# Kernel tuning notes

Measured on AMD Instinct MI355X. Metric: run time of the kernel, lower is better.

The kernel has to match this reference:

```python
import jax, jax.numpy as jnp
import numpy as np

B, N, P, H, BINF = 64, 100, 640000, 128, 11

def setup_inputs() -> dict:
    key = jax.random.key(0)
    ks = jax.random.split(key, 10)
    s = 1.0 / np.sqrt(H)
    sparse_idx = jnp.stack([
        jax.random.randint(ks[0], (P,), 0, B),
        jax.random.randint(ks[1], (P,), 0, N),
        jax.random.randint(ks[2], (P,), 0, N),
    ], axis=1).astype(jnp.int64)  # [P, 3]
    return {
        "local_pair": jax.random.normal(ks[3], (P, H), jnp.float32),
        "global_pair": jax.random.normal(ks[4], (P, H), jnp.float32),
        "binary": jax.random.normal(ks[5], (B, N, N, BINF), jnp.float32),
        "sparse_idx": sparse_idx,
        "W_local": jax.random.normal(ks[6], (H, H), jnp.float32) * s,
        "W_global": jax.random.normal(ks[7], (H, H), jnp.float32) * s,
        "b_global": jnp.zeros((H,), jnp.float32),
        "W_binary": jax.random.normal(ks[8], (BINF, H), jnp.float32) * s,
        "W_score": jax.random.normal(ks[9], (H, 5), jnp.float32) * s,
        "b_score": jnp.zeros((5,), jnp.float32),
    }

def reference(local_pair, global_pair, binary, sparse_idx,
              W_local, W_global, b_global, W_binary, W_score, b_score):
    # gather binary bond features for each scored pair: [P, BINF]
    binary_feats = binary[sparse_idx[:, 0], sparse_idx[:, 1], sparse_idx[:, 2]]
    # fused 3-way linear + relu
    pair_feats = jax.nn.relu(
        local_pair @ W_local
        + (global_pair @ W_global + b_global)
        + binary_feats @ W_binary
    )  # [P, H]
    score = pair_feats @ W_score + b_score  # [P, 5]
    return score
```

## Files before the change

### kernel.cpp

```cpp
#include <hip/hip_runtime.h>
#include <stdint.h>

typedef __bf16 bf16x8 __attribute__((ext_vector_type(8)));
typedef float f32x16 __attribute__((ext_vector_type(16)));

#define H 128
#define NBINF 11
#define NCHUNK 17
#define PTOT 640000
#define ROWS 64
#define NT (PTOT / ROWS)
#define GRID 512
#define ASTRIDE 560
#define ABUF (ROWS * ASTRIDE)
#define FSTRIDE 272

__device__ __align__(16) unsigned short g_wpack[NCHUNK * 4 * 64 * 8];
__device__ __align__(16) unsigned short g_wsp[8 * 64 * 8];
__device__ int g_flag;

__device__ __forceinline__ unsigned short f2bf(float f) {
  return (unsigned short)__builtin_bit_cast(unsigned short, (__bf16)f);
}

__global__ void k_flag(const int* __restrict__ sidx) {
  int t = threadIdx.x;
  int v = sidx[2 * t + 1];
  unsigned long long any = __ballot(v != 0);
  if (t == 0) g_flag = (any == 0ull) ? 2 : 1;
}

__global__ void k_pack(const float* __restrict__ Wl, const float* __restrict__ Wg,
                       const float* __restrict__ Wb, const float* __restrict__ Wsc) {
  int tid = blockIdx.x * 256 + threadIdx.x;
  if (tid < NCHUNK * 4 * 64 * 8) {
    int j = tid & 7, l = (tid >> 3) & 63, nt = (tid >> 9) & 3, c = tid >> 11;
    int k = c * 16 + ((l >> 5) << 3) + j;
    int n = nt * 32 + (l & 31);
    float v = 0.f;
    if (k < 128)       v = Wl[k * H + n];
    else if (k < 256)  v = Wg[(k - 128) * H + n];
    else { int kk = k - 256; v = (kk < NBINF) ? Wb[kk * H + n] : 0.f; }
    g_wpack[tid] = f2bf(v);
  }
  if (tid < 8 * 64 * 8) {
    int j = tid & 7, l = (tid >> 3) & 63, cs = tid >> 9;
    int s = l & 31;
    int k = cs * 16 + ((l >> 5) << 3) + j;
    float v = (s < 5) ? Wsc[k * 5 + s] : 0.f;
    g_wsp[tid] = f2bf(v);
  }
}

__device__ __forceinline__ void bar_lgkm() {
  asm volatile("s_waitcnt lgkmcnt(0)" ::: "memory");
  __builtin_amdgcn_s_barrier();
}

__launch_bounds__(256, 2)
__global__ void k_main(const float* __restrict__ lp, const float* __restrict__ gp,
                       const float* __restrict__ bin, const int* __restrict__ sidx,
                       const float* __restrict__ bg, const float* __restrict__ bsc,
                       float* __restrict__ out) {
  __shared__ __align__(16) char sm[2 * ABUF];
  const int t   = threadIdx.x;
  const int wid = t >> 6;
  const int l   = t & 63;
  const int lr  = l & 31;
  const int lh  = l >> 5;
  const int sflag = g_flag;

  bf16x8 wreg[NCHUNK];
#pragma unroll
  for (int c = 0; c < NCHUNK; ++c)
    wreg[c] = *(const bf16x8*)(g_wpack + ((size_t)(c * 4 + wid) * 64 + l) * 8);
  bf16x8 ws[8];
#pragma unroll
  for (int cs = 0; cs < 8; ++cs)
    ws[cs] = *(const bf16x8*)(g_wsp + ((size_t)cs * 64 + l) * 8);

  const float bgv = bg[wid * 32 + lr];
  const float b0 = bsc[0], b1 = bsc[1], b2 = bsc[2], b3 = bsc[3], b4 = bsc[4];

  float4 pay[16];
  float  bv[8];

  auto issue = [&](int tile) {
    const int p0 = tile * ROWS;
#pragma unroll
    for (int i = 0; i < 8; ++i) {
      int u = t + i * 256, row = u >> 5, slot = u & 31;
      const float* src = (slot < 16)
          ? lp + (size_t)(p0 + row) * H + slot * 8
          : gp + (size_t)(p0 + row) * H + (slot - 16) * 8;
      pay[2 * i]     = ((const float4*)src)[0];
      pay[2 * i + 1] = ((const float4*)src)[1];
    }
    if (t < 2 * ROWS) {
      int row = t >> 1, bh = t & 1, prow = p0 + row;
      int bi = sidx[(prow * 3 + 0) * sflag];
      int ii = sidx[(prow * 3 + 1) * sflag];
      int jj = sidx[(prow * 3 + 2) * sflag];
      int base = ((bi * 100 + ii) * 100 + jj) * NBINF;
#pragma unroll
      for (int j = 0; j < 8; ++j) {
        int e = bh * 8 + j;
        bv[j] = (e < NBINF) ? bin[base + e] : 0.f;
      }
    }
  };

  auto commit = [&](int buf) {
    char* dst = sm + buf * ABUF;
#pragma unroll
    for (int i = 0; i < 8; ++i) {
      int u = t + i * 256, row = u >> 5, slot = u & 31;
      float4 a = pay[2 * i], b = pay[2 * i + 1];
      bf16x8 v;
      v[0] = (__bf16)a.x; v[1] = (__bf16)a.y; v[2] = (__bf16)a.z; v[3] = (__bf16)a.w;
      v[4] = (__bf16)b.x; v[5] = (__bf16)b.y; v[6] = (__bf16)b.z; v[7] = (__bf16)b.w;
      *(bf16x8*)(dst + row * ASTRIDE + slot * 16) = v;
    }
    if (t < 2 * ROWS) {
      int row = t >> 1, bh = t & 1;
      bf16x8 v;
#pragma unroll
      for (int j = 0; j < 8; ++j) v[j] = (__bf16)bv[j];
      *(bf16x8*)(dst + row * ASTRIDE + 512 + bh * 16) = v;
    }
  };

  const int tile0 = blockIdx.x;
  issue(tile0);
  commit(0);
  bar_lgkm();

  int cur = 0;
  for (int tile = tile0; tile < NT; tile += GRID) {
    const int nxt = tile + GRID;
    if (nxt < NT) issue(nxt);

    const char* A = sm + cur * ABUF;
    f32x16 acc[2] = {};
#pragma unroll
    for (int c = 0; c < NCHUNK; ++c) {
#pragma unroll
      for (int rt = 0; rt < 2; ++rt) {
        bf16x8 a = *(const bf16x8*)(A + (rt * 32 + lr) * ASTRIDE + c * 32 + lh * 16);
        acc[rt] = __builtin_amdgcn_mfma_f32_32x32x16_bf16(a, wreg[c], acc[rt], 0, 0, 0);
      }
    }
    bar_lgkm();

    {
      char* F = sm + cur * ABUF;
#pragma unroll
      for (int rt = 0; rt < 2; ++rt) {
#pragma unroll
        for (int rg = 0; rg < 16; ++rg) {
          int rowt = (rg & 3) + ((rg >> 2) << 3) + (lh << 2);
          float fv = fmaxf(acc[rt][rg] + bgv, 0.f);
          *(__bf16*)(F + (size_t)(rt * 32 + rowt) * FSTRIDE +
                     (size_t)(wid * 32 + lr) * 2) = (__bf16)fv;
        }
      }
    }
    bar_lgkm();

    if (wid < 2) {
      const char* F = sm + cur * ABUF;
      f32x16 sacc = {};
#pragma unroll
      for (int cs = 0; cs < 8; ++cs) {
        bf16x8 fb = *(const bf16x8*)(F + (size_t)(wid * 32 + lr) * FSTRIDE +
                                     cs * 32 + lh * 16);
        sacc = __builtin_amdgcn_mfma_f32_32x32x16_bf16(ws[cs], fb, sacc, 0, 0, 0);
      }
      int prow = tile * ROWS + wid * 32 + lr;
      float* op = out + (size_t)prow * 5;
      if (lh == 0) {
        op[0] = sacc[0] + b0; op[1] = sacc[1] + b1;
        op[2] = sacc[2] + b2; op[3] = sacc[3] + b3;
      } else {
        op[4] = sacc[0] + b4;
      }
    }

    if (nxt < NT) commit(cur ^ 1);
    bar_lgkm();
    cur ^= 1;
  }
}

extern "C" void kernel_launch(void* const* d_in, const int* in_sizes, int n_in,
                              void* d_out, int out_size, void* d_ws, size_t ws_size,
                              hipStream_t stream) {
  const float* lp  = (const float*)d_in[0];
  const float* gp  = (const float*)d_in[1];
  const float* bin = (const float*)d_in[2];
  const int*   si  = (const int*)d_in[3];
  const float* Wl  = (const float*)d_in[4];
  const float* Wg  = (const float*)d_in[5];
  const float* bg  = (const float*)d_in[6];
  const float* Wb  = (const float*)d_in[7];
  const float* Wsc = (const float*)d_in[8];
  const float* bsc = (const float*)d_in[9];
  float* out = (float*)d_out;

  hipLaunchKernelGGL(k_flag, dim3(1), dim3(64), 0, stream, si);
  hipLaunchKernelGGL(k_pack, dim3(136), dim3(256), 0, stream, Wl, Wg, Wb, Wsc);
  hipLaunchKernelGGL(k_main, dim3(GRID), dim3(256), 0, stream,
                     lp, gp, bin, si, bg, bsc, out);
}
```

Before: 147.3 us.

## Halve tile rows, prefetch two tiles ahead and split score GEMM across waves

Tiles shrink from 64 to 32 rows. Two register payload sets (A and B) now alternate, so global loads are issued two tiles ahead instead of one. The score projection, which only two waves ran before, is now split across all four waves: each wave computes a K-slice and writes partial sums to LDS, and a final pass reduces them and writes the output. The aim is to keep more memory traffic in flight and balance work across waves. The cost is an extra barrier per tile, an LDS reduction step, and a scattered output store pattern.

```diff
diff --git a/kernel.cpp b/kernel.cpp
--- a/kernel.cpp
+++ b/kernel.cpp
@@ -8,12 +8,13 @@
 #define NBINF 11
 #define NCHUNK 17
 #define PTOT 640000
-#define ROWS 64
+#define ROWS 32
 #define NT (PTOT / ROWS)
 #define GRID 512
 #define ASTRIDE 560
 #define ABUF (ROWS * ASTRIDE)
 #define FSTRIDE 272
+#define PARTOFF 9216
 
 __device__ __align__(16) unsigned short g_wpack[NCHUNK * 4 * 64 * 8];
 __device__ __align__(16) unsigned short g_wsp[8 * 64 * 8];
@@ -74,25 +75,23 @@
 #pragma unroll
   for (int c = 0; c < NCHUNK; ++c)
     wreg[c] = *(const bf16x8*)(g_wpack + ((size_t)(c * 4 + wid) * 64 + l) * 8);
-  bf16x8 ws[8];
-#pragma unroll
-  for (int cs = 0; cs < 8; ++cs)
-    ws[cs] = *(const bf16x8*)(g_wsp + ((size_t)cs * 64 + l) * 8);
+  bf16x8 ws0 = *(const bf16x8*)(g_wsp + ((size_t)(2 * wid + 0) * 64 + l) * 8);
+  bf16x8 ws1 = *(const bf16x8*)(g_wsp + ((size_t)(2 * wid + 1) * 64 + l) * 8);
 
   const float bgv = bg[wid * 32 + lr];
-  const float b0 = bsc[0], b1 = bsc[1], b2 = bsc[2], b3 = bsc[3], b4 = bsc[4];
-
-  float4 pay[16];
-  float  bv[8];
-
-  auto issue = [&](int tile) {
+
+  float4 payA[8]; float bvA[8];
+  float4 payB[8]; float bvB[8];
+
+  auto issue = [&](int tile, float4 (&pay)[8], float (&bv)[8]) {
     const int p0 = tile * ROWS;
 #pragma unroll
-    for (int i = 0; i < 8; ++i) {
-      int u = t + i * 256, row = u >> 5, slot = u & 31;
-      const float* src = (slot < 16)
-          ? lp + (size_t)(p0 + row) * H + slot * 8
-          : gp + (size_t)(p0 + row) * H + (slot - 16) * 8;
+    for (int i = 0; i < 4; ++i) {
+      int v = t + 256 * i;
+      int row = v >> 5, c32 = v & 31;
+      const float* src = (c32 < 16)
+          ? lp + (size_t)(p0 + row) * H + c32 * 8
+          : gp + (size_t)(p0 + row) * H + (c32 - 16) * 8;
       pay[2 * i]     = ((const float4*)src)[0];
       pay[2 * i + 1] = ((const float4*)src)[1];
     }
@@ -110,85 +109,80 @@
     }
   };
 
-  auto commit = [&](int buf) {
-    char* dst = sm + buf * ABUF;
-#pragma unroll
-    for (int i = 0; i < 8; ++i) {
-      int u = t + i * 256, row = u >> 5, slot = u & 31;
+  auto commit = [&](char* dst, float4 (&pay)[8], float (&bv)[8]) {
+#pragma unroll
+    for (int i = 0; i < 4; ++i) {
+      int v = t + 256 * i;
+      int row = v >> 5, c32 = v & 31;
       float4 a = pay[2 * i], b = pay[2 * i + 1];
-      bf16x8 v;
-      v[0] = (__bf16)a.x; v[1] = (__bf16)a.y; v[2] = (__bf16)a.z; v[3] = (__bf16)a.w;
-      v[4] = (__bf16)b.x; v[5] = (__bf16)b.y; v[6] = (__bf16)b.z; v[7] = (__bf16)b.w;
-      *(bf16x8*)(dst + row * ASTRIDE + slot * 16) = v;
+      bf16x8 x;
+      x[0] = (__bf16)a.x; x[1] = (__bf16)a.y; x[2] = (__bf16)a.z; x[3] = (__bf16)a.w;
+      x[4] = (__bf16)b.x; x[5] = (__bf16)b.y; x[6] = (__bf16)b.z; x[7] = (__bf16)b.w;
+      *(bf16x8*)(dst + row * ASTRIDE + c32 * 16) = x;
     }
     if (t < 2 * ROWS) {
       int row = t >> 1, bh = t & 1;
-      bf16x8 v;
-#pragma unroll
-      for (int j = 0; j < 8; ++j) v[j] = (__bf16)bv[j];
-      *(bf16x8*)(dst + row * ASTRIDE + 512 + bh * 16) = v;
+      bf16x8 x;
+#pragma unroll
+      for (int j = 0; j < 8; ++j) x[j] = (__bf16)bv[j];
+      *(bf16x8*)(dst + row * ASTRIDE + 512 + bh * 16) = x;
     }
   };
 
-  const int tile0 = blockIdx.x;
-  issue(tile0);
-  commit(0);
+  auto compute = [&](char* buf, int tile) {
+    f32x16 acc = {};
+#pragma unroll
+    for (int c = 0; c < NCHUNK; ++c) {
+      bf16x8 a = *(const bf16x8*)(buf + lr * ASTRIDE + c * 32 + lh * 16);
+      acc = __builtin_amdgcn_mfma_f32_32x32x16_bf16(a, wreg[c], acc, 0, 0, 0);
+    }
+    bar_lgkm();
+#pragma unroll
+    for (int rg = 0; rg < 16; ++rg) {
+      int p = (rg & 3) + ((rg >> 2) << 3) + (lh << 2);
+      float fv = fmaxf(acc[rg] + bgv, 0.f);
+      *(__bf16*)(buf + (size_t)p * FSTRIDE + (size_t)(wid * 32 + lr) * 2) = (__bf16)fv;
+    }
+    bar_lgkm();
+    f32x16 sacc = {};
+    bf16x8 fb0 = *(const bf16x8*)(buf + (size_t)lr * FSTRIDE + (2 * wid) * 32 + lh * 16);
+    bf16x8 fb1 = *(const bf16x8*)(buf + (size_t)lr * FSTRIDE + (2 * wid + 1) * 32 + lh * 16);
+    sacc = __builtin_amdgcn_mfma_f32_32x32x16_bf16(ws0, fb0, sacc, 0, 0, 0);
+    sacc = __builtin_amdgcn_mfma_f32_32x32x16_bf16(ws1, fb1, sacc, 0, 0, 0);
+    char* part = buf + PARTOFF;
+    if (lh == 0) {
+#pragma unroll
+      for (int s = 0; s < 4; ++s)
+        *(float*)(part + ((size_t)(s * 32 + lr) * 4 + wid) * 4) = sacc[s];
+    } else {
+      *(float*)(part + ((size_t)(4 * 32 + lr) * 4 + wid) * 4) = sacc[0];
+    }
+    bar_lgkm();
+    if (t < 160) {
+      int s = t >> 5, p = t & 31;
+      float4 q = *(const float4*)(part + (size_t)t * 16);
+      out[(size_t)(tile * ROWS + p) * 5 + s] = q.x + q.y + q.z + q.w + bsc[s];
+    }
+  };
+
+  const int t0 = blockIdx.x;
+  issue(t0, payA, bvA);
+  commit(sm, payA, bvA);
+  issue(t0 + GRID, payB, bvB);
   bar_lgkm();
 
-  int cur = 0;
-  for (int tile = tile0; tile < NT; tile += GRID) {
-    const int nxt = tile + GRID;
-    if (nxt < NT) issue(nxt);
-
-    const char* A = sm + cur * ABUF;
-    f32x16 acc[2] = {};
-#pragma unroll
-    for (int c = 0; c < NCHUNK; ++c) {
-#pragma unroll
-      for (int rt = 0; rt < 2; ++rt) {
-        bf16x8 a = *(const bf16x8*)(A + (rt * 32 + lr) * ASTRIDE + c * 32 + lh * 16);
-        acc[rt] = __builtin_amdgcn_mfma_f32_32x32x16_bf16(a, wreg[c], acc[rt], 0, 0, 0);
-      }
-    }
-    bar_lgkm();
-
-    {
-      char* F = sm + cur * ABUF;
-#pragma unroll
-      for (int rt = 0; rt < 2; ++rt) {
-#pragma unroll
-        for (int rg = 0; rg < 16; ++rg) {
-          int rowt = (rg & 3) + ((rg >> 2) << 3) + (lh << 2);
-          float fv = fmaxf(acc[rt][rg] + bgv, 0.f);
-          *(__bf16*)(F + (size_t)(rt * 32 + rowt) * FSTRIDE +
-                     (size_t)(wid * 32 + lr) * 2) = (__bf16)fv;
-        }
-      }
-    }
-    bar_lgkm();
-
-    if (wid < 2) {
-      const char* F = sm + cur * ABUF;
-      f32x16 sacc = {};
-#pragma unroll
-      for (int cs = 0; cs < 8; ++cs) {
-        bf16x8 fb = *(const bf16x8*)(F + (size_t)(wid * 32 + lr) * FSTRIDE +
-                                     cs * 32 + lh * 16);
-        sacc = __builtin_amdgcn_mfma_f32_32x32x16_bf16(ws[cs], fb, sacc, 0, 0, 0);
-      }
-      int prow = tile * ROWS + wid * 32 + lr;
-      float* op = out + (size_t)prow * 5;
-      if (lh == 0) {
-        op[0] = sacc[0] + b0; op[1] = sacc[1] + b1;
-        op[2] = sacc[2] + b2; op[3] = sacc[3] + b3;
-      } else {
-        op[4] = sacc[0] + b4;
-      }
-    }
-
-    if (nxt < NT) commit(cur ^ 1);
-    bar_lgkm();
-    cur ^= 1;
+  for (int u = t0; u < NT; u += 2 * GRID) {
+    const int v = u + GRID;
+    if (u + 2 * GRID < NT) issue(u + 2 * GRID, payA, bvA);
+    compute(sm, u);
+    if (v < NT) commit(sm + ABUF, payB, bvB);
+    bar_lgkm();
+    if (v < NT) {
+      if (v + 2 * GRID < NT) issue(v + 2 * GRID, payB, bvB);
+      compute(sm + ABUF, v);
+      if (u + 2 * GRID < NT) commit(sm, payA, bvA);
+      bar_lgkm();
+    }
   }
 }
 
```

After: 162.8 us. 10.5% more time.
